# Kernel optimization log

Measured on AMD Instinct MI355X. Metric: run time of the kernel, lower is better.

Reference implementation:

```python
import jax, jax.numpy as jnp
import numpy as np

B, S, F, D, H, L, K = 64, 512, 8, 512, 8, 2, 512
FF = 4 * D
DH = D // H


def _ln(x):
    m = jnp.mean(x, axis=-1, keepdims=True)
    v = jnp.var(x, axis=-1, keepdims=True)
    return (x - m) * jax.lax.rsqrt(v + 1e-5)


def _encoder_layer(x, Wqkv, Wo, W1, b1, W2, b2):
    # pre-LN multi-head self-attention
    h = _ln(x)
    qkv = h @ Wqkv                                   # [B,S,3D]
    q, k, v = jnp.split(qkv, 3, axis=-1)
    q = q.reshape(B, S, H, DH)
    k = k.reshape(B, S, H, DH)
    v = v.reshape(B, S, H, DH)
    scores = jnp.einsum('bqhd,bkhd->bhqk', q, k) / jnp.sqrt(jnp.float32(DH))
    attn = jax.nn.softmax(scores, axis=-1)
    o = jnp.einsum('bhqk,bkhd->bqhd', attn, v).reshape(B, S, D) @ Wo
    x = x + o
    # pre-LN feed-forward
    h = _ln(x)
    x = x + (jax.nn.relu(h @ W1 + b1) @ W2 + b2)
    return x


def setup_inputs() -> dict:
    key = jax.random.key(0)
    ks = jax.random.split(key, 12)
    sc = 0.02
    inp = {
        'x': jax.random.normal(ks[0], (B, S, F), dtype=jnp.float32),
        'enc_W': jax.random.normal(ks[1], (F, D), dtype=jnp.float32) * sc,
        'enc_b': jnp.zeros((D,), dtype=jnp.float32),
        'Wqkv': jax.random.normal(ks[2], (L, D, 3 * D), dtype=jnp.float32) * sc,
        'Wo': jax.random.normal(ks[3], (L, D, D), dtype=jnp.float32) * sc,
        'W1': jax.random.normal(ks[4], (L, D, FF), dtype=jnp.float32) * sc,
        'b1': jnp.zeros((L, FF), dtype=jnp.float32),
        'W2': jax.random.normal(ks[5], (L, FF, D), dtype=jnp.float32) * sc,
        'b2': jnp.zeros((L, D), dtype=jnp.float32),
        'centers': jax.random.normal(ks[6], (K, D), dtype=jnp.float32),
    }
    return inp


def reference(x, enc_W, enc_b, Wqkv, Wo, W1, b1, W2, b2, centers):
    # enc_embedding
    h = x @ enc_W + enc_b                            # [B,S,D]
    # seq_model: stack of standard transformer encoder layers
    for i in range(L):
        h = _encoder_layer(h, Wqkv[i], Wo[i], W1[i], b1[i], W2[i], b2[i])
    output_seq = h                                   # [B,S,D]
    # torch.cdist(output_seq, centers, p=2) via matmul expansion
    on2 = jnp.sum(output_seq * output_seq, axis=-1, keepdims=True)   # [B,S,1]
    cn2 = jnp.sum(centers * centers, axis=-1)                        # [K]
    dist2 = on2 + cn2[None, None, :] - 2.0 * jnp.einsum('bsd,kd->bsk', output_seq, centers)
    cluster_ids = jnp.argmin(dist2, axis=-1)                         # [B,S]
    assigned_centroids = centers[cluster_ids]                        # [B,S,D] gather
    diff = output_seq - assigned_centroids
    # torch.norm(diff, dim=1)**2 then mean == mean over (B,D) of sum over S of diff^2
    loss = jnp.mean(jnp.sum(diff * diff, axis=1))
    return loss, output_seq
```

## Files before the change

### kernel.cpp

```cpp
#include <hip/hip_runtime.h>
#include <cstdint>
#include <cstddef>

typedef __attribute__((ext_vector_type(4))) float f32x4;
typedef __attribute__((ext_vector_type(8))) short s16x8;
typedef __attribute__((ext_vector_type(4))) short s16x4;

__device__ __forceinline__ short f2bf(float f){
  unsigned u; __builtin_memcpy(&u, &f, 4);
  u += 0x7fffu + ((u >> 16) & 1u);
  return (short)(u >> 16);
}

__device__ __forceinline__ void gll16(const void* g, void* l) {
  auto* lp = (__attribute__((address_space(3))) unsigned*)(uintptr_t)(l);
  const auto* gp = (const __attribute__((address_space(1))) unsigned*)(uintptr_t)(g);
  __builtin_amdgcn_global_load_lds(gp, lp, 16, 0, 0);
}

__device__ __forceinline__ void ds_tr8(unsigned a, s16x4* r) {
  asm volatile(
    "ds_read_b64_tr_b16 %0, %8\n\t"
    "ds_read_b64_tr_b16 %1, %8 offset:512\n\t"
    "ds_read_b64_tr_b16 %2, %8 offset:2048\n\t"
    "ds_read_b64_tr_b16 %3, %8 offset:2560\n\t"
    "ds_read_b64_tr_b16 %4, %8 offset:4096\n\t"
    "ds_read_b64_tr_b16 %5, %8 offset:4608\n\t"
    "ds_read_b64_tr_b16 %6, %8 offset:6144\n\t"
    "ds_read_b64_tr_b16 %7, %8 offset:6656\n\t"
    "s_waitcnt lgkmcnt(0)"
    : "=&v"(r[0]), "=&v"(r[1]), "=&v"(r[2]), "=&v"(r[3]),
      "=&v"(r[4]), "=&v"(r[5]), "=&v"(r[6]), "=&v"(r[7])
    : "v"(a)
    : "memory");
}

__global__ __launch_bounds__(256) void encode_kernel(
    const float* __restrict__ x, const float* __restrict__ W,
    const float* __restrict__ b, float* __restrict__ out)
{
  const int t = blockIdx.x;
  float xv[8];
#pragma unroll
  for (int f = 0; f < 8; ++f) xv[f] = x[(size_t)t*8 + f];
  for (int d = threadIdx.x; d < 512; d += 256) {
    float acc = b[d];
#pragma unroll
    for (int f = 0; f < 8; ++f) acc += xv[f] * W[f*512 + d];
    out[(size_t)t*512 + d] = acc;
  }
}

__global__ __launch_bounds__(256) void ln_kernel(
    const float* __restrict__ x, short* __restrict__ out)
{
  const int w = threadIdx.x >> 6, lane = threadIdx.x & 63;
  const int t = blockIdx.x * 4 + w;
  const float* row = x + (size_t)t * 512;
  float4 v0 = *(const float4*)&row[lane*8];
  float4 v1 = *(const float4*)&row[lane*8 + 4];
  float vals[8] = {v0.x,v0.y,v0.z,v0.w,v1.x,v1.y,v1.z,v1.w};
  float s = 0.f, sq = 0.f;
#pragma unroll
  for (int i = 0; i < 8; ++i) { s += vals[i]; sq += vals[i]*vals[i]; }
#pragma unroll
  for (int m = 1; m < 64; m <<= 1) { s += __shfl_xor(s, m); sq += __shfl_xor(sq, m); }
  float mean = s * (1.f/512.f);
  float var  = sq * (1.f/512.f) - mean*mean;
  float rstd = rsqrtf(var + 1e-5f);
  s16x8 o;
#pragma unroll
  for (int i = 0; i < 8; ++i) o[i] = f2bf((vals[i]-mean)*rstd);
  *(s16x8*)&out[(size_t)t*512 + lane*8] = o;
}

__global__ __launch_bounds__(256) void transpose_bf16_kernel(
    const float* __restrict__ in, short* __restrict__ out, int K, int N, int kshift)
{
  const int o = blockIdx.x * 256 + threadIdx.x;
  const int k = o & (K - 1), n = o >> kshift;
  out[o] = f2bf(in[(size_t)k * N + n]);
}

__global__ __launch_bounds__(256) void convert_bf16_kernel(
    const float* __restrict__ in, short* __restrict__ out)
{
  const int i = blockIdx.x * 256 + threadIdx.x;
  out[i] = f2bf(in[i]);
}

template<bool BIAS, bool RELU, bool RESID, bool OUT32>
__global__ __launch_bounds__(512, 1) void gemm_kernel(
    const short* __restrict__ A, const short* __restrict__ Bt,
    void* Cout, const float* __restrict__ bias,
    const float* resid, int M, int N, int K)
{
  __shared__ short As[2][256 * 32];
  __shared__ short Bs[2][256 * 32];
  const int tid = threadIdx.x;
  const int lane = tid & 63, w = tid >> 6;
  const int wr = w >> 2, wc = w & 3;
  const int q = lane & 15, g = lane >> 4;

  const int nx = gridDim.x;
  const int d = blockIdx.y * nx + blockIdx.x;
  const int per = (nx * gridDim.y) >> 3;
  const int lid = (d & 7) * per + (d >> 3);
  const int bx = lid % nx, by = lid / nx;
  const int m0 = by * 256, n0 = bx * 256;

  const int srow = lane >> 2;
  const int scol = (((lane & 3) ^ ((lane >> 4) & 3)) * 8);
  const short* aS0 = A  + (size_t)(m0 + w*32 + srow) * K + scol;
  const short* aS1 = aS0 + (size_t)16 * K;
  const short* bS0 = Bt + (size_t)(n0 + w*32 + srow) * K + scol;
  const short* bS1 = bS0 + (size_t)16 * K;
  const int d0 = (w*2) * 512, d1 = (w*2 + 1) * 512;

  const int gs = (g ^ (q >> 2)) * 8;

  f32x4 acc[8][4] = {};
  const int nt = K >> 5;

  gll16(aS0, &As[0][d0]);
  gll16(aS1, &As[0][d1]);
  gll16(bS0, &Bs[0][d0]);
  gll16(bS1, &Bs[0][d1]);
  __syncthreads();

  int cur = 0;
  for (int t = 0; t < nt; ++t) {
    s16x8 aF[8], bF[4];
#pragma unroll
    for (int i = 0; i < 8; ++i) aF[i] = *(const s16x8*)&As[cur][(wr*128 + i*16 + q)*32 + gs];
#pragma unroll
    for (int i = 0; i < 4; ++i) bF[i] = *(const s16x8*)&Bs[cur][(wc*64 + i*16 + q)*32 + gs];
    if (t + 1 < nt) {
      const int k0 = (t + 1) << 5;
      const int nxt = cur ^ 1;
      gll16(aS0 + k0, &As[nxt][d0]);
      gll16(aS1 + k0, &As[nxt][d1]);
      gll16(bS0 + k0, &Bs[nxt][d0]);
      gll16(bS1 + k0, &Bs[nxt][d1]);
    }
    __builtin_amdgcn_sched_barrier(0);
#pragma unroll
    for (int mi = 0; mi < 8; ++mi)
#pragma unroll
      for (int ni = 0; ni < 4; ++ni)
        acc[mi][ni] = __builtin_amdgcn_mfma_f32_16x16x32_bf16(aF[mi], bF[ni], acc[mi][ni], 0, 0, 0);
    __syncthreads();
    cur ^= 1;
  }

#pragma unroll
  for (int mi = 0; mi < 8; ++mi) {
#pragma unroll
    for (int r = 0; r < 4; ++r) {
      const int gr = m0 + wr*128 + mi*16 + g*4 + r;
#pragma unroll
      for (int ni = 0; ni < 4; ++ni) {
        const int gc = n0 + wc*64 + ni*16 + q;
        float v = acc[mi][ni][r];
        if (BIAS) v += bias[gc];
        if (RELU) v = fmaxf(v, 0.f);
        if (RESID) v += resid[(size_t)gr * N + gc];
        if (OUT32) ((float*)Cout)[(size_t)gr * N + gc] = v;
        else       ((short*)Cout)[(size_t)gr * N + gc] = f2bf(v);
      }
    }
  }
}

__global__ __launch_bounds__(256) void attn_kernel(
    const short* __restrict__ qkv, short* __restrict__ attn_out)
{
  __shared__ short Ks[2][64 * 64];
  __shared__ short Vs[2][64 * 64];
  const int tid = threadIdx.x;
  const int w = tid >> 6, lane = tid & 63;
  const int q16 = lane & 15, g = lane >> 4;
  const int dd = blockIdx.x;
  const int lid = (dd & 7) * (int)(gridDim.x >> 3) + (dd >> 3);
  const int qt4 = lid & 7, h = (lid >> 3) & 7, b = lid >> 6;
  const size_t base = (size_t)b * 512 * 1536;
  const int qrow = qt4*64 + w*16 + q16;

  s16x8 bQ0, bQ1;
  {
    const size_t p = base + (size_t)qrow * 1536 + h*64 + g*8;
    bQ0 = *(const s16x8*)&qkv[p];
    bQ1 = *(const s16x8*)&qkv[p + 32];
  }

  const int c0 = w*2, c1 = w*2 + 1;
  const short* kS0 = qkv + base + (size_t)(c0*8 + (lane>>3))*1536 + 512 + h*64 + ((lane&7)^(lane>>3))*8;
  const short* kS1 = qkv + base + (size_t)(c1*8 + (lane>>3))*1536 + 512 + h*64 + ((lane&7)^(lane>>3))*8;
  const short* vS0 = qkv + base + (size_t)((c0&1)*32 + (lane>>1))*1536 + 1024 + h*64 + (c0>>1)*16 + (lane&1)*8;
  const short* vS1 = qkv + base + (size_t)((c1&1)*32 + (lane>>1))*1536 + 1024 + h*64 + (c1>>1)*16 + (lane&1)*8;

  const unsigned vs_lane = (unsigned)(size_t)(&Vs[0][0]) + (unsigned)((q16 + g*64)*2);
  const int sw = q16 & 7;

  float mrun = -1e30f, ssum = 0.f;
  f32x4 O[4] = {};

  gll16(kS0, &Ks[0][c0*512]);
  gll16(kS1, &Ks[0][c1*512]);
  gll16(vS0, &Vs[0][c0*512]);
  gll16(vS1, &Vs[0][c1*512]);
  __syncthreads();

  int cur = 0;
  for (int j0 = 0; j0 < 512; j0 += 64) {
    s16x8 ka0[4], ka1[4];
#pragma unroll
    for (int grp = 0; grp < 4; ++grp) {
      const int rb = (grp*16 + q16) * 64;
      ka0[grp] = *(const s16x8*)&Ks[cur][rb + ((g    ) ^ sw)*8];
      ka1[grp] = *(const s16x8*)&Ks[cur][rb + ((g + 4) ^ sw)*8];
    }
    if (j0 + 64 < 512) {
      const size_t joff = (size_t)(j0 + 64) * 1536;
      const int nxt = cur ^ 1;
      gll16(kS0 + joff, &Ks[nxt][c0*512]);
      gll16(kS1 + joff, &Ks[nxt][c1*512]);
      gll16(vS0 + joff, &Vs[nxt][c0*512]);
      gll16(vS1 + joff, &Vs[nxt][c1*512]);
    }
    __builtin_amdgcn_sched_barrier(0);

    f32x4 c[4];
#pragma unroll
    for (int grp = 0; grp < 4; ++grp) {
      f32x4 z = {};
      c[grp] = __builtin_amdgcn_mfma_f32_16x16x32_bf16(ka0[grp], bQ0, z, 0, 0, 0);
      c[grp] = __builtin_amdgcn_mfma_f32_16x16x32_bf16(ka1[grp], bQ1, c[grp], 0, 0, 0);
    }

    float sc[16];
#pragma unroll
    for (int grp = 0; grp < 4; ++grp)
#pragma unroll
      for (int r = 0; r < 4; ++r) sc[grp*4 + r] = c[grp][r] * 0.125f;
    float bm = sc[0];
#pragma unroll
    for (int i = 1; i < 16; ++i) bm = fmaxf(bm, sc[i]);
    bm = fmaxf(bm, __shfl_xor(bm, 16));
    bm = fmaxf(bm, __shfl_xor(bm, 32));
    const float mn = fmaxf(mrun, bm);
    const float alpha = __expf(mrun - mn);
    float p[16]; float bs = 0.f;
#pragma unroll
    for (int i = 0; i < 16; ++i) { p[i] = __expf(sc[i] - mn); bs += p[i]; }
    bs += __shfl_xor(bs, 16);
    bs += __shfl_xor(bs, 32);
    ssum = ssum * alpha + bs;
    mrun = mn;
#pragma unroll
    for (int db = 0; db < 4; ++db) O[db] *= alpha;

#pragma unroll
    for (int kk = 0; kk < 2; ++kk) {
      s16x8 pf;
#pragma unroll
      for (int e = 0; e < 8; ++e) pf[e] = f2bf(p[(kk*2 + (e >> 2))*4 + (e & 3)]);
      s16x4 r[8];
      ds_tr8(vs_lane + (unsigned)(cur << 13) + (unsigned)(kk*1024), r);
      __builtin_amdgcn_sched_barrier(0);
#pragma unroll
      for (int db = 0; db < 4; ++db) {
        s16x8 vf = __builtin_shufflevector(r[2*db], r[2*db + 1], 0, 1, 2, 3, 4, 5, 6, 7);
        O[db] = __builtin_amdgcn_mfma_f32_16x16x32_bf16(vf, pf, O[db], 0, 0, 0);
      }
    }
    __syncthreads();
    cur ^= 1;
  }

  const float inv = 1.f / ssum;
  const size_t tok = (size_t)b*512 + qrow;
#pragma unroll
  for (int db = 0; db < 4; ++db) {
    s16x4 ov;
#pragma unroll
    for (int r = 0; r < 4; ++r) ov[r] = f2bf(O[db][r] * inv);
    *(s16x4*)&attn_out[tok*512 + h*64 + db*16 + g*4] = ov;
  }
}

__global__ __launch_bounds__(256) void finalize_seq_kernel(
    const float* __restrict__ resid, float* __restrict__ outseq, short* __restrict__ obf)
{
  const size_t i = (size_t)blockIdx.x * 256 + threadIdx.x;
  const float v = resid[i];
  outseq[i] = v;
  obf[i] = f2bf(v);
}

__global__ __launch_bounds__(256) void cn2_kernel(
    const float* __restrict__ centers, float* __restrict__ cn2)
{
  const int c = blockIdx.x;
  __shared__ float red[256];
  float s = 0.f;
  for (int d = threadIdx.x; d < 512; d += 256) { float v = centers[(size_t)c*512 + d]; s += v*v; }
  red[threadIdx.x] = s; __syncthreads();
  for (int off = 128; off > 0; off >>= 1) {
    if (threadIdx.x < off) red[threadIdx.x] += red[threadIdx.x + off];
    __syncthreads();
  }
  if (threadIdx.x == 0) cn2[c] = red[0];
}

__global__ __launch_bounds__(256) void argmin_kernel(
    const float* __restrict__ gdist, const float* __restrict__ cn2,
    const float* __restrict__ resid, const float* __restrict__ centers,
    float* __restrict__ partial)
{
  const int w = threadIdx.x >> 6, lane = threadIdx.x & 63;
  const int t = blockIdx.x * 4 + w;
  float best = 1e30f; int bi = 0;
#pragma unroll
  for (int j = 0; j < 8; ++j) {
    const int k = j*64 + lane;
    const float v = cn2[k] - 2.f * gdist[(size_t)t*512 + k];
    if (v < best || (v == best && k < bi)) { best = v; bi = k; }
  }
#pragma unroll
  for (int mm = 1; mm < 64; mm <<= 1) {
    const float ov = __shfl_xor(best, mm); const int oi = __shfl_xor(bi, mm);
    if (ov < best || (ov == best && oi < bi)) { best = ov; bi = oi; }
  }
  float s = 0.f;
#pragma unroll
  for (int j = 0; j < 2; ++j) {
    float4 o = *(const float4*)&resid[(size_t)t*512 + lane*8 + j*4];
    float4 c = *(const float4*)&centers[(size_t)bi*512 + lane*8 + j*4];
    const float dx = o.x-c.x, dy = o.y-c.y, dz = o.z-c.z, dw = o.w-c.w;
    s += dx*dx + dy*dy + dz*dz + dw*dw;
  }
#pragma unroll
  for (int mm = 1; mm < 64; mm <<= 1) s += __shfl_xor(s, mm);
  __shared__ float red[4];
  if (lane == 0) red[w] = s;
  __syncthreads();
  if (threadIdx.x == 0) partial[blockIdx.x] = red[0] + red[1] + red[2] + red[3];
}

__global__ __launch_bounds__(256) void loss_kernel(
    const float* __restrict__ partial, int n, float* __restrict__ out)
{
  float s = 0.f;
  for (int i = threadIdx.x; i < n; i += 256) s += partial[i];
  __shared__ float red[256];
  red[threadIdx.x] = s; __syncthreads();
  for (int off = 128; off > 0; off >>= 1) {
    if (threadIdx.x < off) red[threadIdx.x] += red[threadIdx.x + off];
    __syncthreads();
  }
  if (threadIdx.x == 0) out[0] = red[0] * (1.f / 32768.f);
}

extern "C" void kernel_launch(void* const* d_in, const int* in_sizes, int n_in,
                              void* d_out, int out_size, void* d_ws, size_t ws_size,
                              hipStream_t stream) {
  const float* x     = (const float*)d_in[0];
  const float* enc_W = (const float*)d_in[1];
  const float* enc_b = (const float*)d_in[2];
  const float* Wqkv  = (const float*)d_in[3];
  const float* Wo    = (const float*)d_in[4];
  const float* W1    = (const float*)d_in[5];
  const float* b1    = (const float*)d_in[6];
  const float* W2    = (const float*)d_in[7];
  const float* b2    = (const float*)d_in[8];
  const float* cen   = (const float*)d_in[9];
  float* out = (float*)d_out;

  const int NT = 32768;
  char* ws = (char*)d_ws;
  float* resid   = (float*)(ws);
  short* h_ln    = (short*)(ws + 67108864);
  char*  pool    = ws + 100663296;
  short* qkv     = (short*)pool;
  short* attn_o  = (short*)(pool + 100663296);
  short* hidden  = (short*)pool;
  float* gdist   = (float*)pool;
  short* wbase   = (short*)(ws + 234881024);
  short* wqT     = wbase;
  short* woT     = wbase + 1572864;
  short* w1T     = wbase + 2097152;
  short* w2T     = wbase + 4194304;
  short* cenb    = wbase + 6291456;
  float* cn2     = (float*)(ws + 247988224);
  float* partial = (float*)(ws + 247990272);

  for (int l = 0; l < 2; ++l) {
    transpose_bf16_kernel<<<3072, 256, 0, stream>>>(Wqkv + (size_t)l*512*1536, wqT + (size_t)l*786432, 512, 1536, 9);
    transpose_bf16_kernel<<<1024, 256, 0, stream>>>(Wo   + (size_t)l*512*512,  woT + (size_t)l*262144, 512, 512, 9);
    transpose_bf16_kernel<<<4096, 256, 0, stream>>>(W1   + (size_t)l*512*2048, w1T + (size_t)l*1048576, 512, 2048, 9);
    transpose_bf16_kernel<<<4096, 256, 0, stream>>>(W2   + (size_t)l*2048*512, w2T + (size_t)l*1048576, 2048, 512, 11);
  }
  convert_bf16_kernel<<<1024, 256, 0, stream>>>(cen, cenb);
  cn2_kernel<<<512, 256, 0, stream>>>(cen, cn2);

  encode_kernel<<<NT, 256, 0, stream>>>(x, enc_W, enc_b, resid);

  for (int l = 0; l < 2; ++l) {
    ln_kernel<<<NT/4, 256, 0, stream>>>(resid, h_ln);
    gemm_kernel<false,false,false,false><<<dim3(6, 128), 512, 0, stream>>>(
        h_ln, wqT + (size_t)l*786432, qkv, nullptr, nullptr, NT, 1536, 512);
    attn_kernel<<<4096, 256, 0, stream>>>(qkv, attn_o);
    gemm_kernel<false,false,true,true><<<dim3(2, 128), 512, 0, stream>>>(
        attn_o, woT + (size_t)l*262144, resid, nullptr, resid, NT, 512, 512);
    ln_kernel<<<NT/4, 256, 0, stream>>>(resid, h_ln);
    gemm_kernel<true,true,false,false><<<dim3(8, 128), 512, 0, stream>>>(
        h_ln, w1T + (size_t)l*1048576, hidden, b1 + (size_t)l*2048, nullptr, NT, 2048, 512);
    gemm_kernel<true,false,true,true><<<dim3(2, 128), 512, 0, stream>>>(
        hidden, w2T + (size_t)l*1048576, resid, b2 + (size_t)l*512, resid, NT, 512, 2048);
  }

  finalize_seq_kernel<<<65536, 256, 0, stream>>>(resid, out + 1, h_ln);
  gemm_kernel<false,false,false,true><<<dim3(2, 128), 512, 0, stream>>>(
      h_ln, cenb, gdist, nullptr, nullptr, NT, 512, 512);
  argmin_kernel<<<NT/4, 256, 0, stream>>>(gdist, cn2, resid, cen, partial);
  loss_kernel<<<1, 256, 0, stream>>>(partial, NT/4, out);
}
```

Measured before the change: 1.039 ms.

## Deepen GEMM LDS pipeline to four stages with counted vmcnt waits

The bf16 MFMA GEMM moves from a double-buffered LDS scheme to four LDS buffers, with tiles prefetched three k-steps ahead. Each iteration now waits only for the oldest outstanding global-to-LDS load group (s_waitcnt vmcnt) and then does a single barrier, instead of a full __syncthreads after every step. The aim is to hide more global-load latency behind the MFMA work and relax synchronisation. In exchange, LDS use per block doubles to 128 KB. Correctness now depends on hand-counted vmcnt values and on barrier placement preventing buffer reuse races.

After: 944.6 us. -9.1%, faster.

```diff
diff --git a/kernel.cpp b/kernel.cpp
--- a/kernel.cpp
+++ b/kernel.cpp
@@ -95,8 +95,8 @@
     void* Cout, const float* __restrict__ bias,
     const float* resid, int M, int N, int K)
 {
-  __shared__ short As[2][256 * 32];
-  __shared__ short Bs[2][256 * 32];
+  __shared__ short As[4][256 * 32];
+  __shared__ short Bs[4][256 * 32];
   const int tid = threadIdx.x;
   const int lane = tid & 63, w = tid >> 6;
   const int wr = w >> 2, wc = w & 3;
@@ -122,36 +122,46 @@
   f32x4 acc[8][4] = {};
   const int nt = K >> 5;
 
-  gll16(aS0, &As[0][d0]);
-  gll16(aS1, &As[0][d1]);
-  gll16(bS0, &Bs[0][d0]);
-  gll16(bS1, &Bs[0][d1]);
-  __syncthreads();
-
-  int cur = 0;
-  for (int t = 0; t < nt; ++t) {
+  auto STAGE = [&](int tt) {
+    const int k0 = tt << 5;
+    const int nb = tt & 3;
+    gll16(aS0 + k0, &As[nb][d0]);
+    gll16(aS1 + k0, &As[nb][d1]);
+    gll16(bS0 + k0, &Bs[nb][d0]);
+    gll16(bS1 + k0, &Bs[nb][d1]);
+  };
+  auto COMPUTE = [&](int t) {
+    const int bufc = t & 3;
+    if (t + 3 < nt) STAGE(t + 3);
     s16x8 aF[8], bF[4];
 #pragma unroll
-    for (int i = 0; i < 8; ++i) aF[i] = *(const s16x8*)&As[cur][(wr*128 + i*16 + q)*32 + gs];
-#pragma unroll
-    for (int i = 0; i < 4; ++i) bF[i] = *(const s16x8*)&Bs[cur][(wc*64 + i*16 + q)*32 + gs];
-    if (t + 1 < nt) {
-      const int k0 = (t + 1) << 5;
-      const int nxt = cur ^ 1;
-      gll16(aS0 + k0, &As[nxt][d0]);
-      gll16(aS1 + k0, &As[nxt][d1]);
-      gll16(bS0 + k0, &Bs[nxt][d0]);
-      gll16(bS1 + k0, &Bs[nxt][d1]);
-    }
-    __builtin_amdgcn_sched_barrier(0);
+    for (int i = 0; i < 8; ++i) aF[i] = *(const s16x8*)&As[bufc][(wr*128 + i*16 + q)*32 + gs];
+#pragma unroll
+    for (int i = 0; i < 4; ++i) bF[i] = *(const s16x8*)&Bs[bufc][(wc*64 + i*16 + q)*32 + gs];
 #pragma unroll
     for (int mi = 0; mi < 8; ++mi)
 #pragma unroll
       for (int ni = 0; ni < 4; ++ni)
         acc[mi][ni] = __builtin_amdgcn_mfma_f32_16x16x32_bf16(aF[mi], bF[ni], acc[mi][ni], 0, 0, 0);
-    __syncthreads();
-    cur ^= 1;
-  }
+  };
+
+  STAGE(0); STAGE(1); STAGE(2);
+
+  for (int t = 0; t < nt - 2; ++t) {
+    asm volatile("s_waitcnt vmcnt(8)" ::: "memory");
+    __builtin_amdgcn_s_barrier();
+    __builtin_amdgcn_sched_barrier(0);
+    COMPUTE(t);
+    __builtin_amdgcn_sched_barrier(0);
+  }
+  asm volatile("s_waitcnt vmcnt(4)" ::: "memory");
+  __builtin_amdgcn_s_barrier();
+  __builtin_amdgcn_sched_barrier(0);
+  COMPUTE(nt - 2);
+  asm volatile("s_waitcnt vmcnt(0)" ::: "memory");
+  __builtin_amdgcn_s_barrier();
+  __builtin_amdgcn_sched_barrier(0);
+  COMPUTE(nt - 1);
 
 #pragma unroll
   for (int mi = 0; mi < 8; ++mi) {
```
